# Performance work log

Measured on AMD Instinct MI355X. Metric: run time of the kernel, lower is better.

Reference implementation:

```python
import jax, jax.numpy as jnp
import numpy as np

B, S, D_IN = 1, 1024, 2048
H_QK, H_V, DK, DV = 8, 16, 128, 128
KCONV = 4
D_OUT = H_QK * DK          # 1024
D_OUT_VG = H_V * DV        # 2048
FUSED = 2 * D_OUT + D_OUT_VG  # 4096
EPS = 1e-6


def setup_inputs() -> dict:
    key = jax.random.key(0)
    ks = jax.random.split(key, 8)
    return {
        "x": jax.random.normal(ks[0], (B, S, D_IN), jnp.float32),
        "w_qkv": jax.random.normal(ks[1], (FUSED, D_IN), jnp.float32) * 0.02,
        "w_gate": jax.random.normal(ks[2], (D_OUT_VG, D_IN), jnp.float32) * 0.02,
        "w_beta": jax.random.normal(ks[3], (H_V, D_IN), jnp.float32) * 0.02,
        "w_alpha": jax.random.normal(ks[4], (H_V, D_IN), jnp.float32) * 0.02,
        "log_A": jnp.log(jax.random.uniform(ks[5], (H_V,), jnp.float32, 1e-3, 16.0)),
        "dt_bias": jnp.ones((H_V,), jnp.float32),
        "conv_w": jax.random.normal(ks[6], (FUSED, 1, KCONV), jnp.float32) * 0.1,
        "rms_w": jnp.ones((DV,), jnp.float32),
        "w_out": jax.random.normal(ks[7], (D_IN, D_OUT_VG), jnp.float32) * 0.02,
    }


def l2_norm(t):
    return t / jnp.sqrt(jnp.sum(t * t, axis=-1, keepdims=True) + EPS)


def rms_norm(t, w):
    var = jnp.mean(t * t, axis=-1, keepdims=True)
    return t * jax.lax.rsqrt(var + EPS) * w


def gated_delta_rule(q, k, v, beta, alpha):
    # q,k: (b,h,s,dk)  v: (b,h,s,dv)  beta,alpha: (b,h,s)
    q = q * (q.shape[-1] ** -0.5)
    S0 = jnp.zeros(q.shape[:2] + (q.shape[-1], v.shape[-1]), q.dtype)

    def step(Sm, inp):
        q_t, k_t, v_t, b_t, a_t = inp  # (b,h,dk) (b,h,dk) (b,h,dv) (b,h) (b,h)
        Sm = Sm * a_t[..., None, None]                      # decay state
        kv = jnp.einsum('bhk,bhkv->bhv', k_t, Sm)           # k^T S
        u = (v_t - kv) * b_t[..., None]                     # delta-rule target
        Sm = Sm + k_t[..., None] * u[:, :, None, :]         # rank-1 update
        o = jnp.einsum('bhk,bhkv->bhv', q_t, Sm)
        return Sm, o

    xs = (jnp.moveaxis(q, 2, 0), jnp.moveaxis(k, 2, 0), jnp.moveaxis(v, 2, 0),
          jnp.moveaxis(beta, 2, 0), jnp.moveaxis(alpha, 2, 0))
    Sf, outs = jax.lax.scan(step, S0, xs)
    return jnp.moveaxis(outs, 0, 2), Sf  # (b,h,s,dv)


def reference(x, w_qkv, w_gate, w_beta, w_alpha, log_A, dt_bias, conv_w, rms_w, w_out):
    b, seq_len, _ = x.shape
    fused_qkv = x @ w_qkv.T                                  # (b,s,FUSED)
    beta = jax.nn.sigmoid(x @ w_beta.T).transpose(0, 2, 1)   # (b,h_v,s)
    token_projs = x @ w_alpha.T                              # (b,s,h_v)
    alpha = jnp.exp(-jnp.exp(log_A) * jax.nn.softplus(token_projs + dt_bias))
    alpha = alpha.transpose(0, 2, 1)                         # (b,h_v,s)

    # causal depthwise conv1d (padding k-1, truncate to seq_len) + SiLU
    conv_in = fused_qkv.transpose(0, 2, 1)                   # (b,C,s)
    conv_out = jax.lax.conv_general_dilated(
        conv_in, conv_w, window_strides=(1,), padding=[(KCONV - 1, 0)],
        dimension_numbers=('NCH', 'OIH', 'NCH'), feature_group_count=FUSED)
    fused_qkv = jax.nn.silu(conv_out).transpose(0, 2, 1)     # (b,s,C)

    query = fused_qkv[..., :D_OUT].reshape(b, seq_len, H_QK, DK).transpose(0, 2, 1, 3)
    key = fused_qkv[..., D_OUT:2 * D_OUT].reshape(b, seq_len, H_QK, DK).transpose(0, 2, 1, 3)
    value = fused_qkv[..., 2 * D_OUT:].reshape(b, seq_len, H_V, DV).transpose(0, 2, 1, 3)

    query, key = l2_norm(query), l2_norm(key)
    rep = H_V // H_QK
    if rep > 1:
        query = jnp.repeat(query, rep, axis=1)
        key = jnp.repeat(key, rep, axis=1)

    ctx, _ = gated_delta_rule(query, key, value, beta, alpha)  # (b,h_v,s,dv)
    ctx = rms_norm(ctx.astype(jnp.float32), rms_w)
    ctx = ctx.transpose(0, 2, 1, 3).reshape(b, seq_len, D_OUT_VG)

    gate = jax.nn.silu(x @ w_gate.T)
    return (gate * ctx) @ w_out.T
```

## Files before the change

kernel.cpp:

```cpp
#include <hip/hip_runtime.h>

#define AS1 __attribute__((address_space(1)))
#define AS3 __attribute__((address_space(3)))

typedef _Float16 f16x8 __attribute__((ext_vector_type(8)));
typedef _Float16 f16x4 __attribute__((ext_vector_type(4)));
typedef _Float16 f16x2 __attribute__((ext_vector_type(2)));
typedef float f32x4 __attribute__((ext_vector_type(4)));

#define MFMA16(a, b, c) __builtin_amdgcn_mfma_f32_16x16x32_f16((a), (b), (c), 0, 0, 0)

__device__ __forceinline__ float silu_f(float v) { return v / (1.f + expf(-v)); }

__device__ __forceinline__ void gload_lds16(const void* g, void* l) {
    __builtin_amdgcn_global_load_lds((AS1 void*)g, (AS3 void*)l, 16, 0, 0);
}

__global__ __launch_bounds__(256) void cvt_proj(const float* __restrict__ x,
                                                const float* __restrict__ w_qkv,
                                                const float* __restrict__ w_gate,
                                                const float* __restrict__ w_out,
                                                _Float16* __restrict__ dst,
                                                const float* __restrict__ w_beta,
                                                const float* __restrict__ w_alpha,
                                                const float* __restrict__ log_A,
                                                const float* __restrict__ dt_bias,
                                                float* __restrict__ betaB,
                                                float* __restrict__ lalphaB) {
    __shared__ float xs[2048];
    const int bid = blockIdx.x, tid = threadIdx.x;
    if (bid < 4608) {
        long base4 = (long)bid * 1024;
        const float* src; long off4;
        if (base4 < 524288)        { src = x;      off4 = 0; }
        else if (base4 < 2621440)  { src = w_qkv;  off4 = 524288; }
        else if (base4 < 3670016)  { src = w_gate; off4 = 2621440; }
        else                       { src = w_out;  off4 = 3670016; }
        const float4* s4 = (const float4*)src + (base4 - off4) + tid;
        float4 v0 = s4[0];
        float4 v1 = s4[256];
        float4 v2 = s4[512];
        float4 v3 = s4[768];
        f16x4* d4 = (f16x4*)dst + base4 + tid;
        f16x4 h0 = { (_Float16)v0.x, (_Float16)v0.y, (_Float16)v0.z, (_Float16)v0.w };
        f16x4 h1 = { (_Float16)v1.x, (_Float16)v1.y, (_Float16)v1.z, (_Float16)v1.w };
        f16x4 h2 = { (_Float16)v2.x, (_Float16)v2.y, (_Float16)v2.z, (_Float16)v2.w };
        f16x4 h3 = { (_Float16)v3.x, (_Float16)v3.y, (_Float16)v3.z, (_Float16)v3.w };
        d4[0]   = h0;
        d4[256] = h1;
        d4[512] = h2;
        d4[768] = h3;
        return;
    }
    const int s = bid - 4608;
    *(float4*)&xs[tid * 8]     = *(const float4*)&x[(long)s * 2048 + tid * 8];
    *(float4*)&xs[tid * 8 + 4] = *(const float4*)&x[(long)s * 2048 + tid * 8 + 4];
    __syncthreads();
    const int o = tid >> 3, j = tid & 7;
    const float* w = (o < 16) ? &w_beta[(long)o * 2048] : &w_alpha[(long)(o - 16) * 2048];
    float p = 0.f;
#pragma unroll 4
    for (int i = 0; i < 64; i++) {
        int d = i * 32 + j * 4;
        float4 wv = *(const float4*)&w[d];
        p += xs[d] * wv.x + xs[d + 1] * wv.y + xs[d + 2] * wv.z + xs[d + 3] * wv.w;
    }
    p += __shfl_xor(p, 1); p += __shfl_xor(p, 2); p += __shfl_xor(p, 4);
    if (j == 0) {
        if (o < 16) {
            betaB[s * 16 + o] = 1.f / (1.f + expf(-p));
        } else {
            int h = o - 16;
            float t = p + dt_bias[h];
            float sp = (t > 20.f) ? t : log1pf(expf(t));
            lalphaB[s * 16 + h] = -expf(log_A[h]) * sp;
        }
    }
}

__global__ __launch_bounds__(256) void gemm_bt128h(const _Float16* __restrict__ A,
                                                   const _Float16* __restrict__ B,
                                                   _Float16* __restrict__ C, int N, int K) {
    __shared__ _Float16 S[3][256 * 32];
    const int tid = threadIdx.x;
    const int rowA0 = blockIdx.y * 128, rowB0 = blockIdx.x * 128;
    const int lane = tid & 63, wv = tid >> 6;
    const int rw = (wv & 1) * 64, cw = (wv >> 1) * 64;
    const int fr = lane & 15, kof = (lane >> 4) * 8, quad = lane >> 4;

    const _Float16* gp[4];
#pragma unroll
    for (int i = 0; i < 4; i++) {
        int idx = tid + 256 * i;
        int row = idx >> 2, c0 = (idx & 3) * 8;
        gp[i] = (row < 128) ? A + (long)(rowA0 + row) * K + c0
                            : B + (long)(rowB0 + row - 128) * K + c0;
    }
    const int NT = K >> 5;

#pragma unroll
    for (int i = 0; i < 4; i++) gload_lds16(gp[i], &S[0][(tid + 256 * i) * 8]);
#pragma unroll
    for (int i = 0; i < 4; i++) gload_lds16(gp[i] + 32, &S[1][(tid + 256 * i) * 8]);
    asm volatile("s_waitcnt vmcnt(4)" ::: "memory");
    __builtin_amdgcn_s_barrier();

    f32x4 zero = {0.f, 0.f, 0.f, 0.f};
    f32x4 acc[4][4];
#pragma unroll
    for (int mi = 0; mi < 4; mi++)
#pragma unroll
        for (int ni = 0; ni < 4; ni++) acc[mi][ni] = zero;

    int cur = 0;
    for (int t = 0; t < NT; ++t) {
        if (t + 2 < NT) {
            int nb = cur + 2; if (nb >= 3) nb -= 3;
#pragma unroll
            for (int i = 0; i < 4; i++)
                gload_lds16(gp[i] + (t + 2) * 32, &S[nb][(tid + 256 * i) * 8]);
        }
        f16x8 af[4], bf[4];
#pragma unroll
        for (int mi = 0; mi < 4; mi++)
            af[mi] = *(const f16x8*)&S[cur][(rw + mi * 16 + fr) * 32 + kof];
#pragma unroll
        for (int ni = 0; ni < 4; ni++)
            bf[ni] = *(const f16x8*)&S[cur][(128 + cw + ni * 16 + fr) * 32 + kof];
#pragma unroll
        for (int mi = 0; mi < 4; mi++)
#pragma unroll
            for (int ni = 0; ni < 4; ni++)
                acc[mi][ni] = MFMA16(af[mi], bf[ni], acc[mi][ni]);
        if (t + 2 < NT) { asm volatile("s_waitcnt vmcnt(4)" ::: "memory"); }
        else            { asm volatile("s_waitcnt vmcnt(0)" ::: "memory"); }
        __builtin_amdgcn_s_barrier();
        cur = (cur == 2) ? 0 : cur + 1;
    }
    const int rbase = quad * 4;
#pragma unroll
    for (int mi = 0; mi < 4; mi++)
#pragma unroll
        for (int ni = 0; ni < 4; ni++) {
            int row = rowA0 + rw + mi * 16 + rbase;
            int col = rowB0 + cw + ni * 16 + fr;
#pragma unroll
            for (int r = 0; r < 4; r++)
                C[(long)(row + r) * N + col] = (_Float16)acc[mi][ni][r];
        }
}

__global__ __launch_bounds__(256) void gemm_bt6464(const _Float16* __restrict__ A,
                                                   const _Float16* __restrict__ B,
                                                   float* __restrict__ C, int N, int K) {
    __shared__ _Float16 S[3][128 * 32];
    const int tid = threadIdx.x;
    const int rowA0 = blockIdx.y * 64, rowB0 = blockIdx.x * 64;
    const int lane = tid & 63, wv = tid >> 6;
    const int rw = (wv & 1) * 32, cwol = (wv >> 1) * 32;
    const int fr = lane & 15, kof = (lane >> 4) * 8, quad = lane >> 4;

    const _Float16* gp[2];
#pragma unroll
    for (int i = 0; i < 2; i++) {
        int idx = tid + 256 * i;
        int row = idx >> 2, c0 = (idx & 3) * 8;
        gp[i] = (row < 64) ? A + (long)(rowA0 + row) * K + c0
                           : B + (long)(rowB0 + row - 64) * K + c0;
    }
    const int NT = K >> 5;

#pragma unroll
    for (int i = 0; i < 2; i++) gload_lds16(gp[i], &S[0][(tid + 256 * i) * 8]);
#pragma unroll
    for (int i = 0; i < 2; i++) gload_lds16(gp[i] + 32, &S[1][(tid + 256 * i) * 8]);
    asm volatile("s_waitcnt vmcnt(2)" ::: "memory");
    __builtin_amdgcn_s_barrier();

    f32x4 zero = {0.f, 0.f, 0.f, 0.f};
    f32x4 acc[2][2];
#pragma unroll
    for (int mi = 0; mi < 2; mi++)
#pragma unroll
        for (int ni = 0; ni < 2; ni++) acc[mi][ni] = zero;

    int cur = 0;
    for (int t = 0; t < NT; ++t) {
        if (t + 2 < NT) {
            int nb = cur + 2; if (nb >= 3) nb -= 3;
#pragma unroll
            for (int i = 0; i < 2; i++)
                gload_lds16(gp[i] + (t + 2) * 32, &S[nb][(tid + 256 * i) * 8]);
        }
        f16x8 af[2], bf[2];
#pragma unroll
        for (int mi = 0; mi < 2; mi++)
            af[mi] = *(const f16x8*)&S[cur][(rw + mi * 16 + fr) * 32 + kof];
#pragma unroll
        for (int ni = 0; ni < 2; ni++)
            bf[ni] = *(const f16x8*)&S[cur][(64 + cwol + ni * 16 + fr) * 32 + kof];
#pragma unroll
        for (int mi = 0; mi < 2; mi++)
#pragma unroll
            for (int ni = 0; ni < 2; ni++)
                acc[mi][ni] = MFMA16(af[mi], bf[ni], acc[mi][ni]);
        if (t + 2 < NT) { asm volatile("s_waitcnt vmcnt(2)" ::: "memory"); }
        else            { asm volatile("s_waitcnt vmcnt(0)" ::: "memory"); }
        __builtin_amdgcn_s_barrier();
        cur = (cur == 2) ? 0 : cur + 1;
    }
    const int rbase = quad * 4;
#pragma unroll
    for (int mi = 0; mi < 2; mi++)
#pragma unroll
        for (int ni = 0; ni < 2; ni++) {
            int row = rowA0 + rw + mi * 16 + rbase;
            int col = rowB0 + cwol + ni * 16 + fr;
#pragma unroll
            for (int r = 0; r < 4; r++)
                C[(long)(row + r) * N + col] = acc[mi][ni][r];
        }
}

__global__ __launch_bounds__(512) void chunk_front(const _Float16* __restrict__ pre,
                                                   const float* __restrict__ cw,
                                                   const float* __restrict__ betaB,
                                                   const float* __restrict__ lalphaB,
                                                   _Float16* __restrict__ Mw,
                                                   _Float16* __restrict__ QTw,
                                                   _Float16* __restrict__ KTw,
                                                   _Float16* __restrict__ WTw,
                                                   _Float16* __restrict__ Bw,
                                                   _Float16* __restrict__ BTw,
                                                   float* __restrict__ gamC) {
    __shared__ _Float16 Kh[64 * 136];
    __shared__ _Float16 Qh[64 * 136];
    __shared__ _Float16 Vh[64 * 136];
    __shared__ _Float16 Tl[64 * 72];
    __shared__ float lg[64], betL[64], bgamL[64], egQ[64], egKr[64];
    const int hc = blockIdx.x, h = hc >> 4, c = hc & 15, hq = h >> 1, s0 = c * 64;
    const int tid = threadIdx.x;

    if (tid < 64) {
        float la = lalphaB[(s0 + tid) * 16 + h];
#pragma unroll
        for (int d = 1; d < 64; d <<= 1) {
            float tv = __shfl_up(la, d, 64);
            if (tid >= d) la += tv;
        }
        lg[tid] = la;
        float la63 = __shfl(la, 63, 64);
        float b = betaB[(s0 + tid) * 16 + h];
        float eg = expf(la);
        betL[tid] = b;
        bgamL[tid] = b * eg;
        egQ[tid] = eg;
        egKr[tid] = expf(la63 - la);
        if (tid == 63) gamC[hc] = eg;
    }

    {
        const int tt = tid >> 3, pp = tid & 7, m0 = pp * 16;
        const _Float16* rp[4];
        bool ok0, ok1, ok2;
        {
            int sb = s0 + tt - 3;
            ok0 = (sb >= 0); ok1 = (sb + 1 >= 0); ok2 = (sb + 2 >= 0);
            rp[0] = pre + (long)sb * 6144;
            rp[1] = pre + (long)(sb + 1) * 6144;
            rp[2] = pre + (long)(sb + 2) * 6144;
            rp[3] = pre + (long)(sb + 3) * 6144;
        }
#pragma unroll
        for (int sel = 0; sel < 3; sel++) {
            const int colbase = (sel == 0) ? hq * 128 : (sel == 1) ? 1024 + hq * 128
                                                                   : 2048 + h * 128;
            float vals[16];
            float ss = 0.f;
#pragma unroll
            for (int g = 0; g < 2; g++) {
                const int co = colbase + m0 + g * 8;
                f16x8 r0 = {}, r1 = {}, r2 = {}, r3;
                if (ok0) r0 = *(const f16x8*)&rp[0][co];
                if (ok1) r1 = *(const f16x8*)&rp[1][co];
                if (ok2) r2 = *(const f16x8*)&rp[2][co];
                r3 = *(const f16x8*)&rp[3][co];
#pragma unroll
                for (int j = 0; j < 8; j++) {
                    float4 w = *(const float4*)&cw[(co + j) * 4];
                    float a = (float)r0[j] * w.x + (float)r1[j] * w.y +
                              (float)r2[j] * w.z + (float)r3[j] * w.w;
                    a = silu_f(a);
                    vals[g * 8 + j] = a;
                    ss += a * a;
                }
            }
            float sc = 1.f;
            if (sel < 2) {
                ss += __shfl_xor(ss, 1); ss += __shfl_xor(ss, 2); ss += __shfl_xor(ss, 4);
                sc = rsqrtf(ss + 1e-6f);
                if (sel == 0) sc *= 0.08838834764831843f;
            }
            _Float16* dst = (sel == 0) ? Qh : (sel == 1) ? Kh : Vh;
#pragma unroll
            for (int g = 0; g < 2; g++) {
                f16x8 hv;
#pragma unroll
                for (int j = 0; j < 8; j++) hv[j] = (_Float16)(vals[g * 8 + j] * sc);
                *(f16x8*)&dst[tt * 136 + m0 + g * 8] = hv;
            }
        }
    }
    __syncthreads();

    const int wv = tid >> 6, lane = tid & 63;
    const int fr = lane & 15, kof = (lane >> 4) * 8, quad = lane >> 4;
    {
        f32x4 zero = {0.f, 0.f, 0.f, 0.f};
        if (wv < 4) {
            f32x4 accT[4];
#pragma unroll
            for (int ci = 0; ci < 4; ci++) accT[ci] = zero;
            for (int k0 = 0; k0 < 128; k0 += 32) {
                f16x8 ak = *(const f16x8*)&Kh[(wv * 16 + fr) * 136 + k0 + kof];
#pragma unroll
                for (int ci = 0; ci < 4; ci++)
                    accT[ci] = MFMA16(ak, *(const f16x8*)&Kh[(ci * 16 + fr) * 136 + k0 + kof], accT[ci]);
            }
#pragma unroll
            for (int ci = 0; ci < 4; ci++)
#pragma unroll
                for (int r = 0; r < 4; r++) {
                    int t = wv * 16 + quad * 4 + r, i = ci * 16 + fr;
                    float e = expf(lg[t] - lg[i]);
                    Tl[t * 72 + i] = (_Float16)((i < t) ? betL[t] * e * accT[ci][r] : 0.f);
                }
        } else {
            const int w = wv - 4;
            f32x4 accM[4];
#pragma unroll
            for (int ci = 0; ci < 4; ci++) accM[ci] = zero;
            for (int k0 = 0; k0 < 128; k0 += 32) {
                f16x8 aq = *(const f16x8*)&Qh[(w * 16 + fr) * 136 + k0 + kof];
#pragma unroll
                for (int ci = 0; ci < 4; ci++)
                    accM[ci] = MFMA16(aq, *(const f16x8*)&Kh[(ci * 16 + fr) * 136 + k0 + kof], accM[ci]);
            }
#pragma unroll
            for (int ci = 0; ci < 4; ci++)
#pragma unroll
                for (int r = 0; r < 4; r++) {
                    int t = w * 16 + quad * 4 + r, i = ci * 16 + fr;
                    float e = expf(lg[t] - lg[i]);
                    Mw[(long)hc * 4096 + t * 64 + i] = (_Float16)((i <= t) ? e * accM[ci][r] : 0.f);
                }
        }
    }
    __syncthreads();

    if (wv < 4) {
        const int jcol = tid & 127;
        const _Float16* Xsrc = (wv < 2) ? Vh : Kh;
        const float* dscale = (wv < 2) ? betL : bgamL;
        float Xs[64];
#pragma unroll
        for (int t = 0; t < 64; t++) Xs[t] = dscale[t] * (float)Xsrc[t * 136 + jcol];
#pragma unroll
        for (int a = 0; a < 4; a++) {
#pragma unroll
            for (int b = 0; b < a; b++) {
#pragma unroll
                for (int r = 0; r < 16; r++) {
                    const _Float16* trow = &Tl[(a * 16 + r) * 72 + b * 16];
                    f16x8 t0 = *(const f16x8*)trow;
                    f16x8 t1 = *(const f16x8*)(trow + 8);
                    float acc = 0.f;
#pragma unroll
                    for (int k = 0; k < 8; k++) acc += (float)t0[k] * Xs[b * 16 + k];
#pragma unroll
                    for (int k = 0; k < 8; k++) acc += (float)t1[k] * Xs[b * 16 + 8 + k];
                    Xs[a * 16 + r] -= acc;
                }
            }
#pragma unroll
            for (int sp = 1; sp < 16; sp++) {
                const _Float16* trow = &Tl[(a * 16 + sp) * 72 + a * 16];
                f16x8 t0 = *(const f16x8*)trow;
                f16x8 t1 = *(const f16x8*)(trow + 8);
                float acc = 0.f;
#pragma unroll
                for (int tp = 0; tp < 16; tp++) {
                    if (tp < sp) acc += (float)(tp < 8 ? t0[tp] : t1[tp - 8]) * Xs[a * 16 + tp];
                }
                Xs[a * 16 + sp] -= acc;
            }
        }
        if (wv < 2) {
#pragma unroll
            for (int v = 0; v < 8; v++) {
                f16x8 hv;
#pragma unroll
                for (int j = 0; j < 8; j++) hv[j] = (_Float16)Xs[v * 8 + j];
                *(f16x8*)&WTw[((long)hc * 128 + jcol) * 64 + v * 8] = hv;
            }
        } else {
#pragma unroll
            for (int t = 0; t < 64; t++) Bw[(long)hc * 8192 + t * 128 + jcol] = (_Float16)Xs[t];
#pragma unroll
            for (int v = 0; v < 8; v++) {
                f16x8 hv;
#pragma unroll
                for (int j = 0; j < 8; j++) hv[j] = (_Float16)Xs[v * 8 + j];
                *(f16x8*)&BTw[((long)hc * 128 + jcol) * 64 + v * 8] = hv;
            }
        }
    } else {
        const int w = wv - 4;
#pragma unroll
        for (int cp = 0; cp < 4; cp++) {
            int t = w * 16 + fr;
            int cc = cp * 32 + kof;
            f16x8 q = *(const f16x8*)&Qh[t * 136 + cc];
            float s = egQ[t];
            f16x8 o;
#pragma unroll
            for (int j = 0; j < 8; j++) o[j] = (_Float16)(s * (float)q[j]);
            *(f16x8*)&QTw[(long)hc * 8192 + t * 128 + cc] = o;
        }
        const int m = w * 32 + (lane & 31);
        const int tb = (lane >> 5) * 8;
#pragma unroll
        for (int tp = 0; tp < 4; tp++) {
            int t0 = tb + tp * 16;
            f16x8 o;
#pragma unroll
            for (int j = 0; j < 8; j++)
                o[j] = (_Float16)(egKr[t0 + j] * (float)Kh[(t0 + j) * 136 + m]);
            *(f16x8*)&KTw[(long)hc * 8192 + m * 64 + t0] = o;
        }
    }
}

__global__ __launch_bounds__(256) void gr_kernel(const _Float16* __restrict__ KTw,
                                                 const _Float16* __restrict__ BTw,
                                                 const _Float16* __restrict__ WTw,
                                                 _Float16* __restrict__ Gw,
                                                 float* __restrict__ Rtw) {
    __shared__ _Float16 KTl[128 * 72], BTl[128 * 72], WTl[128 * 72];
    const long hc = blockIdx.x;
    const int tid = threadIdx.x;
    {
        int r = tid >> 1, c0 = (tid & 1) * 32;
        const _Float16* k_ = &KTw[hc * 8192 + r * 64 + c0];
        const _Float16* b_ = &BTw[hc * 8192 + r * 64 + c0];
        const _Float16* w_ = &WTw[hc * 8192 + r * 64 + c0];
#pragma unroll
        for (int i = 0; i < 4; i++) {
            *(f16x8*)&KTl[r * 72 + c0 + i * 8] = *(const f16x8*)&k_[i * 8];
            *(f16x8*)&BTl[r * 72 + c0 + i * 8] = *(const f16x8*)&b_[i * 8];
            *(f16x8*)&WTl[r * 72 + c0 + i * 8] = *(const f16x8*)&w_[i * 8];
        }
    }
    __syncthreads();
    const int wv = tid >> 6, lane = tid & 63;
    const int fr = lane & 15, kof = (lane >> 4) * 8, quad = lane >> 4;
    f32x4 zero = {0.f, 0.f, 0.f, 0.f};
#pragma unroll
    for (int mi = 0; mi < 2; mi++) {
        int m0 = (wv * 2 + mi) * 16;
        f16x8 a0 = *(const f16x8*)&KTl[(m0 + fr) * 72 + kof];
        f16x8 a1 = *(const f16x8*)&KTl[(m0 + fr) * 72 + 32 + kof];
#pragma unroll
        for (int nj = 0; nj < 8; nj++) {
            f32x4 acc = zero;
            acc = MFMA16(a0, *(const f16x8*)&BTl[(nj * 16 + fr) * 72 + kof], acc);
            acc = MFMA16(a1, *(const f16x8*)&BTl[(nj * 16 + fr) * 72 + 32 + kof], acc);
#pragma unroll
            for (int r = 0; r < 4; r++)
                Gw[hc * 16384 + (long)(m0 + quad * 4 + r) * 128 + nj * 16 + fr] = (_Float16)acc[r];
        }
    }
#pragma unroll
    for (int ji = 0; ji < 2; ji++) {
        int j0 = (wv * 2 + ji) * 16;
        f16x8 a0 = *(const f16x8*)&WTl[(j0 + fr) * 72 + kof];
        f16x8 a1 = *(const f16x8*)&WTl[(j0 + fr) * 72 + 32 + kof];
#pragma unroll
        for (int nm = 0; nm < 8; nm++) {
            f32x4 acc = zero;
            acc = MFMA16(a0, *(const f16x8*)&KTl[(nm * 16 + fr) * 72 + kof], acc);
            acc = MFMA16(a1, *(const f16x8*)&KTl[(nm * 16 + fr) * 72 + 32 + kof], acc);
#pragma unroll
            for (int r = 0; r < 4; r++)
                Rtw[hc * 16384 + (long)(j0 + quad * 4 + r) * 128 + nm * 16 + fr] = acc[r];
        }
    }
}

__global__ __launch_bounds__(256) void serial_scan(const _Float16* __restrict__ Gw,
                                                   const float* __restrict__ Rtw,
                                                   const float* __restrict__ gamC,
                                                   float* __restrict__ Zdump) {
    __shared__ _Float16 Zhi[32 * 136], Zlo[32 * 136];
    __shared__ _Float16 Gl[128 * 136];
    const int tid = threadIdx.x;
    const int h = blockIdx.x >> 2, js = (blockIdx.x & 3) * 32;
    const int wv = tid >> 6, lane = tid & 63;
    const int fr = lane & 15, kof = (lane >> 4) * 8, quad = lane >> 4;
    const int gr_ = tid >> 1, gc_ = (tid & 1) * 64;

    for (int e = tid; e < 32 * 136; e += 256) { Zhi[e] = (_Float16)0.f; Zlo[e] = (_Float16)0.f; }
    float z[2][2][4];
#pragma unroll
    for (int jt = 0; jt < 2; jt++)
#pragma unroll
        for (int u = 0; u < 2; u++)
#pragma unroll
            for (int r = 0; r < 4; r++) z[jt][u][r] = 0.f;

    long hc0 = (long)h * 16;
    f16x8 gpre[8];
#pragma unroll
    for (int i = 0; i < 8; i++)
        gpre[i] = *(const f16x8*)&Gw[hc0 * 16384 + (long)gr_ * 128 + gc_ + i * 8];
    float rpre[2][2][4];
#pragma unroll
    for (int jt = 0; jt < 2; jt++)
#pragma unroll
        for (int u = 0; u < 2; u++)
#pragma unroll
            for (int r = 0; r < 4; r++)
                rpre[jt][u][r] = Rtw[hc0 * 16384 +
                                     (long)(js + jt * 16 + quad * 4 + r) * 128 +
                                     (2 * wv + u) * 16 + fr];
    __syncthreads();

    for (int c = 0; c < 16; ++c) {
        long hc = (long)h * 16 + c;
        float gC = gamC[hc];
#pragma unroll
        for (int i = 0; i < 8; i++)
            *(f16x8*)&Gl[gr_ * 136 + gc_ + i * 8] = gpre[i];
        long hcn = (long)h * 16 + (c < 15 ? c + 1 : 15);
        f16x8 gnext[8];
#pragma unroll
        for (int i = 0; i < 8; i++)
            gnext[i] = *(const f16x8*)&Gw[hcn * 16384 + (long)gr_ * 128 + gc_ + i * 8];
        float rnext[2][2][4];
#pragma unroll
        for (int jt = 0; jt < 2; jt++)
#pragma unroll
            for (int u = 0; u < 2; u++)
#pragma unroll
                for (int r = 0; r < 4; r++)
                    rnext[jt][u][r] = Rtw[hcn * 16384 +
                                          (long)(js + jt * 16 + quad * 4 + r) * 128 +
                                          (2 * wv + u) * 16 + fr];
        __syncthreads();
        f32x4 acc[2][2];
        f32x4 zero = {0.f, 0.f, 0.f, 0.f};
#pragma unroll
        for (int jt = 0; jt < 2; jt++)
#pragma unroll
            for (int u = 0; u < 2; u++) acc[jt][u] = zero;
        for (int k0 = 0; k0 < 128; k0 += 32) {
            f16x8 ahi[2], alo[2], bfr[2];
#pragma unroll
            for (int jt = 0; jt < 2; jt++) {
                ahi[jt] = *(const f16x8*)&Zhi[(jt * 16 + fr) * 136 + k0 + kof];
                alo[jt] = *(const f16x8*)&Zlo[(jt * 16 + fr) * 136 + k0 + kof];
            }
#pragma unroll
            for (int u = 0; u < 2; u++)
                bfr[u] = *(const f16x8*)&Gl[((2 * wv + u) * 16 + fr) * 136 + k0 + kof];
#pragma unroll
            for (int jt = 0; jt < 2; jt++)
#pragma unroll
                for (int u = 0; u < 2; u++) {
                    acc[jt][u] = MFMA16(ahi[jt], bfr[u], acc[jt][u]);
                    acc[jt][u] = MFMA16(alo[jt], bfr[u], acc[jt][u]);
                }
        }
        __syncthreads();
#pragma unroll
        for (int jt = 0; jt < 2; jt++)
#pragma unroll
            for (int u = 0; u < 2; u++)
#pragma unroll
                for (int r = 0; r < 4; r++) {
                    int j = jt * 16 + quad * 4 + r;
                    int m = (2 * wv + u) * 16 + fr;
                    Zdump[hc * 16384 + (long)(js + j) * 128 + m] = z[jt][u][r];
                    float zn = gC * z[jt][u][r] - acc[jt][u][r] + rpre[jt][u][r];
                    z[jt][u][r] = zn;
                    _Float16 hi = (_Float16)zn;
                    Zhi[j * 136 + m] = hi;
                    Zlo[j * 136 + m] = (_Float16)(zn - (float)hi);
                }
#pragma unroll
        for (int i = 0; i < 8; i++) gpre[i] = gnext[i];
#pragma unroll
        for (int jt = 0; jt < 2; jt++)
#pragma unroll
            for (int u = 0; u < 2; u++)
#pragma unroll
                for (int r = 0; r < 4; r++) rpre[jt][u][r] = rnext[jt][u][r];
    }
}

__global__ __launch_bounds__(256) void out_chunk(const float* __restrict__ Zdump,
                                                 const _Float16* __restrict__ Bw,
                                                 const _Float16* __restrict__ WTw,
                                                 const _Float16* __restrict__ QTw,
                                                 const _Float16* __restrict__ Mw,
                                                 float* __restrict__ ctx) {
    __shared__ _Float16 SThi[64 * 136], STlo[64 * 136], Bl[64 * 136];
    __shared__ _Float16 UT[64 * 72];
    const int bid = blockIdx.x;
    const long hc = bid >> 1;
    const int jh = (bid & 1) * 64;
    const int h = (int)(hc >> 4), c = (int)(hc & 15), s0 = c * 64;
    const int tid = threadIdx.x, wv = tid >> 6, lane = tid & 63;
    const int fr = lane & 15, kof = (lane >> 4) * 8, quad = lane >> 4;
    {
        int r = tid >> 2, c0 = (tid & 3) * 32;
        const float* src = &Zdump[hc * 16384 + (long)(jh + r) * 128 + c0];
#pragma unroll
        for (int i = 0; i < 8; i++) {
            float4 v = *(const float4*)&src[i * 4];
            _Float16 h0 = (_Float16)v.x, h1 = (_Float16)v.y, h2 = (_Float16)v.z, h3 = (_Float16)v.w;
            f16x4 hi = {h0, h1, h2, h3};
            f16x4 lo = {(_Float16)(v.x - (float)h0), (_Float16)(v.y - (float)h1),
                        (_Float16)(v.z - (float)h2), (_Float16)(v.w - (float)h3)};
            *(f16x4*)&SThi[r * 136 + c0 + i * 4] = hi;
            *(f16x4*)&STlo[r * 136 + c0 + i * 4] = lo;
        }
        const _Float16* bsrc = &Bw[hc * 8192 + r * 128 + c0];
#pragma unroll
        for (int i = 0; i < 4; i++)
            *(f16x8*)&Bl[r * 136 + c0 + i * 8] = *(const f16x8*)&bsrc[i * 8];
    }
    __syncthreads();
    const int t0 = wv * 16;
    f16x8 ba[4];
#pragma unroll
    for (int k = 0; k < 4; k++)
        ba[k] = *(const f16x8*)&Bl[(t0 + fr) * 136 + k * 32 + kof];
#pragma unroll
    for (int jt = 0; jt < 4; jt++) {
        f32x4 acc = {0.f, 0.f, 0.f, 0.f};
#pragma unroll
        for (int k = 0; k < 4; k++) {
            acc = MFMA16(ba[k], *(const f16x8*)&SThi[(jt * 16 + fr) * 136 + k * 32 + kof], acc);
            acc = MFMA16(ba[k], *(const f16x8*)&STlo[(jt * 16 + fr) * 136 + k * 32 + kof], acc);
        }
#pragma unroll
        for (int r = 0; r < 4; r++) {
            int t = t0 + quad * 4 + r;
            int j = jt * 16 + fr;
            float w = (float)WTw[hc * 8192 + (long)(jh + j) * 64 + t];
            UT[j * 72 + t] = (_Float16)(w - acc[r]);
        }
    }
    __syncthreads();
    f16x8 qa[4], ma[2];
#pragma unroll
    for (int k = 0; k < 4; k++)
        qa[k] = *(const f16x8*)&QTw[hc * 8192 + (long)(t0 + fr) * 128 + k * 32 + kof];
#pragma unroll
    for (int k = 0; k < 2; k++)
        ma[k] = *(const f16x8*)&Mw[hc * 4096 + (long)(t0 + fr) * 64 + k * 32 + kof];
#pragma unroll
    for (int jt = 0; jt < 4; jt++) {
        f32x4 acc = {0.f, 0.f, 0.f, 0.f};
#pragma unroll
        for (int k = 0; k < 4; k++) {
            acc = MFMA16(qa[k], *(const f16x8*)&SThi[(jt * 16 + fr) * 136 + k * 32 + kof], acc);
            acc = MFMA16(qa[k], *(const f16x8*)&STlo[(jt * 16 + fr) * 136 + k * 32 + kof], acc);
        }
#pragma unroll
        for (int k = 0; k < 2; k++)
            acc = MFMA16(ma[k], *(const f16x8*)&UT[(jt * 16 + fr) * 72 + k * 32 + kof], acc);
#pragma unroll
        for (int r = 0; r < 4; r++) {
            int t = t0 + quad * 4 + r;
            int j = jt * 16 + fr;
            ctx[(long)(s0 + t) * 2048 + h * 128 + jh + j] = acc[r];
        }
    }
}

__global__ void epilogue_k(const float* __restrict__ ctx, const _Float16* __restrict__ pre,
                           const float* __restrict__ rms_w, _Float16* __restrict__ y) {
    int gw = (blockIdx.x * blockDim.x + threadIdx.x) >> 6;
    int lane = threadIdx.x & 63;
    int s = gw >> 4, h = gw & 15;
    long base = (long)s * 2048 + h * 128;
    long gbase = (long)s * 6144 + 4096 + h * 128;
    float2 cv = *(const float2*)&ctx[base + lane * 2];
    float ss = cv.x * cv.x + cv.y * cv.y;
#pragma unroll
    for (int m = 1; m < 64; m <<= 1) ss += __shfl_xor(ss, m);
    float sc = rsqrtf(ss * (1.f / 128.f) + 1e-6f);
    int d = lane * 2;
    float2 rw = *(const float2*)&rms_w[d];
    f16x2 gv = *(const f16x2*)&pre[gbase + d];
    float g0 = silu_f((float)gv[0]);
    float g1 = silu_f((float)gv[1]);
    f16x2 hv = { (_Float16)(cv.x * sc * rw.x * g0), (_Float16)(cv.y * sc * rw.y * g1) };
    *(f16x2*)&y[base + d] = hv;
}

extern "C" void kernel_launch(void* const* d_in, const int* in_sizes, int n_in,
                              void* d_out, int out_size, void* d_ws, size_t ws_size,
                              hipStream_t stream) {
    const float* x       = (const float*)d_in[0];
    const float* w_qkv   = (const float*)d_in[1];
    const float* w_gate  = (const float*)d_in[2];
    const float* w_beta  = (const float*)d_in[3];
    const float* w_alpha = (const float*)d_in[4];
    const float* log_A   = (const float*)d_in[5];
    const float* dt_bias = (const float*)d_in[6];
    const float* conv_w  = (const float*)d_in[7];
    const float* rms_w   = (const float*)d_in[8];
    const float* w_out   = (const float*)d_in[9];
    float* outp = (float*)d_out;

    char* ws = (char*)d_ws;
    size_t off = 0;
    _Float16* xb     = (_Float16*)(ws + off); off += (size_t)1024 * 2048 * 2;
    _Float16* wfused = (_Float16*)(ws + off); off += (size_t)6144 * 2048 * 2;
    _Float16* woutb  = (_Float16*)(ws + off); off += (size_t)2048 * 2048 * 2;
    _Float16* yb     = (_Float16*)(ws + off); off += (size_t)1024 * 2048 * 2;
    _Float16* pre    = (_Float16*)(ws + off); off += (size_t)1024 * 6144 * 2;
    float* ctx       = (float*)(ws + off);    off += (size_t)1024 * 16 * 128 * 4;
    float* betaB     = (float*)(ws + off);    off += (size_t)1024 * 16 * 4;
    float* lalphaB   = (float*)(ws + off);    off += (size_t)1024 * 16 * 4;
    _Float16* Mw     = (_Float16*)(ws + off); off += (size_t)256 * 4096 * 2;
    _Float16* QTw    = (_Float16*)(ws + off); off += (size_t)256 * 8192 * 2;
    _Float16* KTw    = (_Float16*)(ws + off); off += (size_t)256 * 8192 * 2;
    _Float16* WTw    = (_Float16*)(ws + off); off += (size_t)256 * 8192 * 2;
    _Float16* Bw     = (_Float16*)(ws + off); off += (size_t)256 * 8192 * 2;
    _Float16* BTw    = (_Float16*)(ws + off); off += (size_t)256 * 8192 * 2;
    float* gamC      = (float*)(ws + off);    off += (size_t)256 * 4;
    _Float16* Gw     = (_Float16*)(ws + off); off += (size_t)256 * 16384 * 2;
    float* Rtw       = (float*)(ws + off);    off += (size_t)256 * 16384 * 4;
    float* Zdump     = (float*)(ws + off);    off += (size_t)256 * 16384 * 4;

    cvt_proj<<<5632, 256, 0, stream>>>(x, w_qkv, w_gate, w_out, xb,
                                       w_beta, w_alpha, log_A, dt_bias, betaB, lalphaB);

    gemm_bt128h<<<dim3(48, 8), 256, 0, stream>>>(xb, wfused, pre, 6144, 2048);

    chunk_front<<<256, 512, 0, stream>>>(pre, conv_w, betaB, lalphaB,
                                         Mw, QTw, KTw, WTw, Bw, BTw, gamC);
    gr_kernel<<<256, 256, 0, stream>>>(KTw, BTw, WTw, Gw, Rtw);
    serial_scan<<<64, 256, 0, stream>>>(Gw, Rtw, gamC, Zdump);
    out_chunk<<<512, 256, 0, stream>>>(Zdump, Bw, WTw, QTw, Mw, ctx);

    epilogue_k<<<4096, 256, 0, stream>>>(ctx, pre, rms_w, yb);
    gemm_bt6464<<<dim3(32, 16), 256, 0, stream>>>(yb, woutb, outp, 2048, 2048);
}
```

Before: 271.5 us.

## Fuse chunk output computation with RMSNorm and gating epilogue

Merges the out_chunk kernel and the separate epilogue kernel into a single 512-thread block per head-chunk that covers both 64-column halves of the value dimension. The row sum of squares for RMSNorm is reduced in registers and through shared memory across the two halves, and the gated, normalized half-precision output is written directly. This removes the fp32 ctx round trip through global memory and one kernel launch. In exchange it halves the grid size, raises shared memory per block, and the final stores become scalar and less coalesced.

New measurement: 271.0 us. No clear change (-0.2%).

```diff
diff --git a/kernel.cpp b/kernel.cpp
--- a/kernel.cpp
+++ b/kernel.cpp
@@ -608,23 +608,26 @@
     }
 }
 
-__global__ __launch_bounds__(256) void out_chunk(const float* __restrict__ Zdump,
+__global__ __launch_bounds__(512) void out_fused(const float* __restrict__ Zdump,
                                                  const _Float16* __restrict__ Bw,
                                                  const _Float16* __restrict__ WTw,
                                                  const _Float16* __restrict__ QTw,
                                                  const _Float16* __restrict__ Mw,
-                                                 float* __restrict__ ctx) {
-    __shared__ _Float16 SThi[64 * 136], STlo[64 * 136], Bl[64 * 136];
-    __shared__ _Float16 UT[64 * 72];
-    const int bid = blockIdx.x;
-    const long hc = bid >> 1;
-    const int jh = (bid & 1) * 64;
+                                                 const _Float16* __restrict__ pre,
+                                                 const float* __restrict__ rms_w,
+                                                 _Float16* __restrict__ y) {
+    __shared__ _Float16 SThi[128 * 136], STlo[128 * 136];
+    __shared__ _Float16 Bl[64 * 136];
+    __shared__ _Float16 UT[2][64 * 72];
+    __shared__ float rowsq[2][64];
+    const long hc = blockIdx.x;
     const int h = (int)(hc >> 4), c = (int)(hc & 15), s0 = c * 64;
     const int tid = threadIdx.x, wv = tid >> 6, lane = tid & 63;
+    const int half = wv >> 2, wvh = wv & 3, jh = half * 64;
     const int fr = lane & 15, kof = (lane >> 4) * 8, quad = lane >> 4;
     {
         int r = tid >> 2, c0 = (tid & 3) * 32;
-        const float* src = &Zdump[hc * 16384 + (long)(jh + r) * 128 + c0];
+        const float* src = &Zdump[hc * 16384 + (long)r * 128 + c0];
 #pragma unroll
         for (int i = 0; i < 8; i++) {
             float4 v = *(const float4*)&src[i * 4];
@@ -635,13 +638,16 @@
             *(f16x4*)&SThi[r * 136 + c0 + i * 4] = hi;
             *(f16x4*)&STlo[r * 136 + c0 + i * 4] = lo;
         }
-        const _Float16* bsrc = &Bw[hc * 8192 + r * 128 + c0];
-#pragma unroll
-        for (int i = 0; i < 4; i++)
-            *(f16x8*)&Bl[r * 136 + c0 + i * 8] = *(const f16x8*)&bsrc[i * 8];
+        if (tid < 256) {
+            int r2 = tid >> 2, cb = (tid & 3) * 32;
+            const _Float16* bsrc = &Bw[hc * 8192 + r2 * 128 + cb];
+#pragma unroll
+            for (int i = 0; i < 4; i++)
+                *(f16x8*)&Bl[r2 * 136 + cb + i * 8] = *(const f16x8*)&bsrc[i * 8];
+        }
     }
     __syncthreads();
-    const int t0 = wv * 16;
+    const int t0 = wvh * 16;
     f16x8 ba[4];
 #pragma unroll
     for (int k = 0; k < 4; k++)
@@ -651,15 +657,15 @@
         f32x4 acc = {0.f, 0.f, 0.f, 0.f};
 #pragma unroll
         for (int k = 0; k < 4; k++) {
-            acc = MFMA16(ba[k], *(const f16x8*)&SThi[(jt * 16 + fr) * 136 + k * 32 + kof], acc);
-            acc = MFMA16(ba[k], *(const f16x8*)&STlo[(jt * 16 + fr) * 136 + k * 32 + kof], acc);
+            acc = MFMA16(ba[k], *(const f16x8*)&SThi[(jh + jt * 16 + fr) * 136 + k * 32 + kof], acc);
+            acc = MFMA16(ba[k], *(const f16x8*)&STlo[(jh + jt * 16 + fr) * 136 + k * 32 + kof], acc);
         }
 #pragma unroll
         for (int r = 0; r < 4; r++) {
             int t = t0 + quad * 4 + r;
             int j = jt * 16 + fr;
             float w = (float)WTw[hc * 8192 + (long)(jh + j) * 64 + t];
-            UT[j * 72 + t] = (_Float16)(w - acc[r]);
+            UT[half][j * 72 + t] = (_Float16)(w - acc[r]);
         }
     }
     __syncthreads();
@@ -670,45 +676,49 @@
 #pragma unroll
     for (int k = 0; k < 2; k++)
         ma[k] = *(const f16x8*)&Mw[hc * 4096 + (long)(t0 + fr) * 64 + k * 32 + kof];
+    f32x4 out[4];
 #pragma unroll
     for (int jt = 0; jt < 4; jt++) {
         f32x4 acc = {0.f, 0.f, 0.f, 0.f};
 #pragma unroll
         for (int k = 0; k < 4; k++) {
-            acc = MFMA16(qa[k], *(const f16x8*)&SThi[(jt * 16 + fr) * 136 + k * 32 + kof], acc);
-            acc = MFMA16(qa[k], *(const f16x8*)&STlo[(jt * 16 + fr) * 136 + k * 32 + kof], acc);
+            acc = MFMA16(qa[k], *(const f16x8*)&SThi[(jh + jt * 16 + fr) * 136 + k * 32 + kof], acc);
+            acc = MFMA16(qa[k], *(const f16x8*)&STlo[(jh + jt * 16 + fr) * 136 + k * 32 + kof], acc);
         }
 #pragma unroll
         for (int k = 0; k < 2; k++)
-            acc = MFMA16(ma[k], *(const f16x8*)&UT[(jt * 16 + fr) * 72 + k * 32 + kof], acc);
-#pragma unroll
-        for (int r = 0; r < 4; r++) {
-            int t = t0 + quad * 4 + r;
+            acc = MFMA16(ma[k], *(const f16x8*)&UT[half][(jt * 16 + fr) * 72 + k * 32 + kof], acc);
+        out[jt] = acc;
+    }
+    float pr[4];
+#pragma unroll
+    for (int r = 0; r < 4; r++) {
+        float s = 0.f;
+#pragma unroll
+        for (int jt = 0; jt < 4; jt++) s += out[jt][r] * out[jt][r];
+        s += __shfl_xor(s, 1); s += __shfl_xor(s, 2);
+        s += __shfl_xor(s, 4); s += __shfl_xor(s, 8);
+        pr[r] = s;
+    }
+    if (fr == 0) {
+#pragma unroll
+        for (int r = 0; r < 4; r++) rowsq[half][t0 + quad * 4 + r] = pr[r];
+    }
+    __syncthreads();
+#pragma unroll
+    for (int r = 0; r < 4; r++) {
+        int t = t0 + quad * 4 + r;
+        float ss = rowsq[0][t] + rowsq[1][t];
+        float sc = rsqrtf(ss * (1.f / 128.f) + 1e-6f);
+        long rb = (long)(s0 + t) * 6144 + 4096 + h * 128 + jh;
+        long yb_ = (long)(s0 + t) * 2048 + h * 128 + jh;
+#pragma unroll
+        for (int jt = 0; jt < 4; jt++) {
             int j = jt * 16 + fr;
-            ctx[(long)(s0 + t) * 2048 + h * 128 + jh + j] = acc[r];
-        }
-    }
-}
-
-__global__ void epilogue_k(const float* __restrict__ ctx, const _Float16* __restrict__ pre,
-                           const float* __restrict__ rms_w, _Float16* __restrict__ y) {
-    int gw = (blockIdx.x * blockDim.x + threadIdx.x) >> 6;
-    int lane = threadIdx.x & 63;
-    int s = gw >> 4, h = gw & 15;
-    long base = (long)s * 2048 + h * 128;
-    long gbase = (long)s * 6144 + 4096 + h * 128;
-    float2 cv = *(const float2*)&ctx[base + lane * 2];
-    float ss = cv.x * cv.x + cv.y * cv.y;
-#pragma unroll
-    for (int m = 1; m < 64; m <<= 1) ss += __shfl_xor(ss, m);
-    float sc = rsqrtf(ss * (1.f / 128.f) + 1e-6f);
-    int d = lane * 2;
-    float2 rw = *(const float2*)&rms_w[d];
-    f16x2 gv = *(const f16x2*)&pre[gbase + d];
-    float g0 = silu_f((float)gv[0]);
-    float g1 = silu_f((float)gv[1]);
-    f16x2 hv = { (_Float16)(cv.x * sc * rw.x * g0), (_Float16)(cv.y * sc * rw.y * g1) };
-    *(f16x2*)&y[base + d] = hv;
+            float g = silu_f((float)pre[rb + j]);
+            y[yb_ + j] = (_Float16)(out[jt][r] * sc * rms_w[jh + j] * g);
+        }
+    }
 }
 
 extern "C" void kernel_launch(void* const* d_in, const int* in_sizes, int n_in,
@@ -733,7 +743,6 @@
     _Float16* woutb  = (_Float16*)(ws + off); off += (size_t)2048 * 2048 * 2;
     _Float16* yb     = (_Float16*)(ws + off); off += (size_t)1024 * 2048 * 2;
     _Float16* pre    = (_Float16*)(ws + off); off += (size_t)1024 * 6144 * 2;
-    float* ctx       = (float*)(ws + off);    off += (size_t)1024 * 16 * 128 * 4;
     float* betaB     = (float*)(ws + off);    off += (size_t)1024 * 16 * 4;
     float* lalphaB   = (float*)(ws + off);    off += (size_t)1024 * 16 * 4;
     _Float16* Mw     = (_Float16*)(ws + off); off += (size_t)256 * 4096 * 2;
@@ -756,8 +765,8 @@
                                          Mw, QTw, KTw, WTw, Bw, BTw, gamC);
     gr_kernel<<<256, 256, 0, stream>>>(KTw, BTw, WTw, Gw, Rtw);
     serial_scan<<<64, 256, 0, stream>>>(Gw, Rtw, gamC, Zdump);
-    out_chunk<<<512, 256, 0, stream>>>(Zdump, Bw, WTw, QTw, Mw, ctx);
-
-    epilogue_k<<<4096, 256, 0, stream>>>(ctx, pre, rms_w, yb);
+
+    out_fused<<<256, 512, 0, stream>>>(Zdump, Bw, WTw, QTw, Mw, pre, rms_w, yb);
+
     gemm_bt6464<<<dim3(32, 16), 256, 0, stream>>>(yb, woutb, outp, 2048, 2048);
 }
```
